# Performance work log

Hardware: AMD Instinct MI355X
Metric: run time of the kernel (lower is better)

The kernel has to match this reference:

```python
import jax, jax.numpy as jnp
import numpy as np

N_NODES = 50000
N_EDGES = 600000  # incidence entries; hyperedge ids also live in [0, N_NODES)
HID = 128


def _prelu(x, a):
    return jnp.where(x >= 0, x, a * x)


def _hypergraph_conv(x, W, b, node_idx, edge_idx, num_nodes, num_hedges):
    # PyG HypergraphConv (use_attention=False, heads=1):
    # out = D^{-1} H B^{-1} H^T (X Theta) + bias
    xw = x @ W  # [N, F]
    ones = jnp.ones(node_idx.shape[0], dtype=x.dtype)
    D = jax.ops.segment_sum(ones, node_idx, num_segments=num_nodes)   # node degree
    B = jax.ops.segment_sum(ones, edge_idx, num_segments=num_hedges)  # hyperedge degree
    Dinv = jnp.where(D > 0, 1.0 / D, 0.0)
    Binv = jnp.where(B > 0, 1.0 / B, 0.0)
    # node -> hyperedge aggregation, scaled by B^{-1}
    m = jax.ops.segment_sum(xw[node_idx], edge_idx, num_segments=num_hedges) * Binv[:, None]
    # hyperedge -> node aggregation, scaled by D^{-1}
    out = jax.ops.segment_sum(m[edge_idx], node_idx, num_segments=num_nodes) * Dinv[:, None]
    return out + b


def setup_inputs() -> dict:
    key = jax.random.key(0)
    k1, k2, k3, k4, k5 = jax.random.split(key, 5)
    x = jax.random.normal(k1, (N_NODES, HID), dtype=jnp.float32)
    hyper_edge_index = jax.random.randint(k2, (2, N_EDGES), 0, N_NODES, dtype=jnp.int64)
    # kaiming-normal-ish linear weights, zero biases (per init_weights)
    std = float(np.sqrt(2.0 / HID))
    W1 = jax.random.normal(k3, (HID, HID), dtype=jnp.float32) * std
    W2 = jax.random.normal(k4, (HID, HID), dtype=jnp.float32) * std
    b1 = jnp.zeros((HID,), dtype=jnp.float32)
    b2 = jnp.zeros((HID,), dtype=jnp.float32)
    prelu_a = jnp.full((1,), 0.25, dtype=jnp.float32)  # nn.PReLU default
    return {"x": x, "hyper_edge_index": hyper_edge_index,
            "W1": W1, "b1": b1, "W2": W2, "b2": b2, "prelu_a": prelu_a}


def reference(x, hyper_edge_index, W1, b1, W2, b2, prelu_a):
    node_idx = hyper_edge_index[0]
    edge_idx = hyper_edge_index[1]
    h = _hypergraph_conv(x, W1, b1, node_idx, edge_idx, N_NODES, N_NODES)
    h = _prelu(h, prelu_a)
    h = _hypergraph_conv(h, W2, b2, node_idx, edge_idx, N_NODES, N_NODES)
    h = h + x  # residual
    return _prelu(h, prelu_a)
```

## Files before the change

kernel.cpp:

```cpp
#include <hip/hip_runtime.h>

typedef unsigned short u16;
typedef unsigned int   u32;
typedef unsigned long long u64;

#define HID 128
#define KPB 256
#define NBMAX 512
#define IPB 2048
#define CAP 6144

typedef __bf16 bf16x8 __attribute__((ext_vector_type(8)));
typedef float  f32x4  __attribute__((ext_vector_type(4)));

__device__ inline float u2f(u32 u){ union{u32 u;float f;} v; v.u=u; return v.f; }
__device__ inline u32   f2u(float f){ union{float f;u32 u;} v; v.f=f; return v.u; }
__device__ inline u32  f2bfu(float f){ u32 b=f2u(f); return ((b + 0x7FFFu + ((b>>16)&1u))>>16)&0xFFFFu; }
__device__ inline float blo(u32 u){ return u2f(u<<16); }
__device__ inline float bhi(u32 u){ return u2f(u & 0xFFFF0000u); }
__device__ inline u32  pk(float lo, float hi){ return (f2bfu(hi)<<16) | f2bfu(lo); }

__global__ __launch_bounds__(256) void k_wfrag2(const float* __restrict__ W1, const float* __restrict__ W2,
                                                u16* __restrict__ W1f, u16* __restrict__ W2f){
    int gid = blockIdx.x*256 + threadIdx.x;
    const float* W = (gid < 16384) ? W1 : W2;
    u16* Wf = (gid < 16384) ? W1f : W2f;
    int id = gid & 16383;
    int i = id & 7, l = (id>>3)&63, j = (id>>9)&7, s = id>>12;
    int k = s*32 + ((l>>4)<<3) + i;
    int n = (j<<4) + (l&15);
    Wf[id] = (u16)f2bfu(W[k*HID + n]);
}

__global__ __launch_bounds__(256) void k_hist(const int* __restrict__ nidx, const int* __restrict__ eidx,
                                              int* __restrict__ hist, int nE, int nN, int nb){
    __shared__ int h[NBMAX];
    for (int t=threadIdx.x; t<nb; t+=256) h[t]=0;
    __syncthreads();
    int base = blockIdx.x*IPB;
    for (int k=threadIdx.x; k<IPB; k+=256){
        int j = base+k;
        if (j < nE){
            int n = nidx[j], e = eidx[j];
            atomicAdd(&h[n>>8], 1);
            atomicAdd(&h[(nN+e)>>8], 1);
        }
    }
    __syncthreads();
    for (int t=threadIdx.x; t<nb; t+=256) if (h[t]) atomicAdd(&hist[t], h[t]);
}

__global__ __launch_bounds__(256) void k_bscan(const int* __restrict__ hist, int* __restrict__ bbase,
                                               int* __restrict__ bfill, int* __restrict__ off,
                                               int nb, int nkeys, int total){
    __shared__ int sd[256];
    int t = threadIdx.x;
    int c0 = (2*t   < nb) ? hist[2*t]   : 0;
    int c1 = (2*t+1 < nb) ? hist[2*t+1] : 0;
    int s = c0 + c1;
    sd[t] = s; __syncthreads();
    for (int o=1;o<256;o<<=1){ int u = (t>=o)? sd[t-o] : 0; __syncthreads(); sd[t]+=u; __syncthreads(); }
    int ex = sd[t] - s;
    if (2*t   < nb){ bbase[2*t]   = ex;      bfill[2*t]   = ex; }
    if (2*t+1 < nb){ bbase[2*t+1] = ex+c0;   bfill[2*t+1] = ex+c0; }
    if (t == 0){ bbase[nb] = total; off[nkeys] = total; }
}

__global__ __launch_bounds__(256) void k_part(const int* __restrict__ nidx, const int* __restrict__ eidx,
                                              int* __restrict__ bfill, u64* __restrict__ pairs,
                                              int nE, int nN, int nb){
    __shared__ int h[NBMAX], rsv[NBMAX], fl[NBMAX];
    for (int t=threadIdx.x; t<nb; t+=256){ h[t]=0; fl[t]=0; }
    __syncthreads();
    int base = blockIdx.x*IPB;
    for (int k=threadIdx.x; k<IPB; k+=256){
        int j = base+k;
        if (j < nE){
            int n = nidx[j], e = eidx[j];
            atomicAdd(&h[n>>8], 1);
            atomicAdd(&h[(nN+e)>>8], 1);
        }
    }
    __syncthreads();
    for (int t=threadIdx.x; t<nb; t+=256){ if (h[t]) rsv[t] = atomicAdd(&bfill[t], h[t]); }
    __syncthreads();
    for (int k=threadIdx.x; k<IPB; k+=256){
        int j = base+k;
        if (j < nE){
            int n = nidx[j], e = eidx[j];
            int b1 = n>>8;
            int p1 = rsv[b1] + atomicAdd(&fl[b1], 1);
            pairs[p1] = ((u64)(u32)n << 32) | (u32)e;
            int k2 = nN + e;
            int b2 = k2>>8;
            int p2 = rsv[b2] + atomicAdd(&fl[b2], 1);
            pairs[p2] = ((u64)(u32)k2 << 32) | (u32)n;
        }
    }
}

__global__ __launch_bounds__(256) void k_bucket(const u64* __restrict__ pairs, const int* __restrict__ bbase,
                                                int* __restrict__ csr, int* __restrict__ off, int nkeys){
    __shared__ int cntS[KPB];
    __shared__ int fillS[KPB];
    __shared__ int vals[CAP];
    int b = blockIdx.x;
    int t = threadIdx.x;
    int base = bbase[b];
    int n = bbase[b+1] - base;
    int k0 = b * KPB;

    cntS[t] = 0;
    __syncthreads();
    for (int i=t; i<n; i+=256){
        u64 p = pairs[base+i];
        int kl = (int)(p>>32) - k0;
        atomicAdd(&cntS[kl], 1);
    }
    __syncthreads();
    int c = cntS[t];
    __syncthreads();
    fillS[t] = c; __syncthreads();
    for (int o=1;o<256;o<<=1){ int u = (t>=o)? fillS[t-o] : 0; __syncthreads(); fillS[t]+=u; __syncthreads(); }
    int ex = fillS[t] - c;
    __syncthreads();
    cntS[t] = ex; fillS[t] = ex;
    __syncthreads();
    int k = k0 + t;
    if (k < nkeys) off[k] = base + ex;
    bool fits = (n <= CAP);
    for (int i=t; i<n; i+=256){
        u64 p = pairs[base+i];
        int kl = (int)(p>>32) - k0;
        int pos = atomicAdd(&fillS[kl], 1);
        if (fits) vals[pos] = (int)(u32)p;
        else      csr[base+pos] = (int)(u32)p;
    }
    __syncthreads();
    if (fits){
        for (int i=t; i<n; i+=256) csr[base+i] = vals[i];
    }
}

__global__ __launch_bounds__(256) void k_gemm(const u16* __restrict__ A, const u16* __restrict__ Wf,
                                              u16* __restrict__ C, int M){
    int wave = blockIdx.x*4 + (threadIdx.x>>6);
    int lane = threadIdx.x & 63;
    int rtiles = M >> 4;
    if (wave >= rtiles) return;
    int row0 = wave << 4;

    const u16* Arow = A + (size_t)(row0 + (lane&15))*HID + ((lane>>4)<<3);
    const bf16x8* Wp = reinterpret_cast<const bf16x8*>(Wf) + lane;

    f32x4 acc[8];
    #pragma unroll
    for (int j=0;j<8;++j) acc[j] = (f32x4){0.f,0.f,0.f,0.f};

    #pragma unroll
    for (int s=0;s<4;++s){
        bf16x8 a = *reinterpret_cast<const bf16x8*>(Arow + s*32);
        #pragma unroll
        for (int j=0;j<8;++j){
            bf16x8 b = Wp[(s*8 + j)*64];
            acc[j] = __builtin_amdgcn_mfma_f32_16x16x32_bf16(a, b, acc[j], 0, 0, 0);
        }
    }
    int r0 = row0 + ((lane>>4)<<2);
    int c0 = lane & 15;
    #pragma unroll
    for (int j=0;j<8;++j){
        #pragma unroll
        for (int r=0;r<4;++r){
            C[(size_t)(r0+r)*HID + j*16 + c0] = (u16)f2bfu(acc[j][r]);
        }
    }
}

__global__ __launch_bounds__(256) void k_gemm_f32(const float* __restrict__ A, const u16* __restrict__ Wf,
                                                  u16* __restrict__ C, int M){
    int wave = blockIdx.x*4 + (threadIdx.x>>6);
    int lane = threadIdx.x & 63;
    int rtiles = M >> 4;
    if (wave >= rtiles) return;
    int row0 = wave << 4;

    const float* Arow = A + (size_t)(row0 + (lane&15))*HID + ((lane>>4)<<3);
    const bf16x8* Wp = reinterpret_cast<const bf16x8*>(Wf) + lane;

    f32x4 acc[8];
    #pragma unroll
    for (int j=0;j<8;++j) acc[j] = (f32x4){0.f,0.f,0.f,0.f};

    #pragma unroll
    for (int s=0;s<4;++s){
        float4 f0 = *reinterpret_cast<const float4*>(Arow + s*32);
        float4 f1 = *reinterpret_cast<const float4*>(Arow + s*32 + 4);
        union { u16 h[8]; bf16x8 v; } au;
        au.h[0]=(u16)f2bfu(f0.x); au.h[1]=(u16)f2bfu(f0.y); au.h[2]=(u16)f2bfu(f0.z); au.h[3]=(u16)f2bfu(f0.w);
        au.h[4]=(u16)f2bfu(f1.x); au.h[5]=(u16)f2bfu(f1.y); au.h[6]=(u16)f2bfu(f1.z); au.h[7]=(u16)f2bfu(f1.w);
        #pragma unroll
        for (int j=0;j<8;++j){
            bf16x8 b = Wp[(s*8 + j)*64];
            acc[j] = __builtin_amdgcn_mfma_f32_16x16x32_bf16(au.v, b, acc[j], 0, 0, 0);
        }
    }
    int r0 = row0 + ((lane>>4)<<2);
    int c0 = lane & 15;
    #pragma unroll
    for (int j=0;j<8;++j){
        #pragma unroll
        for (int r=0;r<4;++r){
            C[(size_t)(r0+r)*HID + j*16 + c0] = (u16)f2bfu(acc[j][r]);
        }
    }
}

template<int MODE>
__global__ __launch_bounds__(256) void k_agg(const u32* __restrict__ tab, const int* __restrict__ csr,
                                             const int* __restrict__ off, void* __restrict__ outp,
                                             const float* __restrict__ bias, const float* __restrict__ resid,
                                             const float* __restrict__ aptr, int nrows){
    int d = blockIdx.x*4 + (threadIdx.x>>6);
    if (d >= nrows) return;
    int lane = threadIdx.x & 63;
    int g = lane >> 4;
    int c = lane & 15;
    int start = off[d], end = off[d+1];
    int deg = end - start;

    int myc = 0;
    if (lane < deg) myc = csr[start + lane];

    float a0=0.f,a1=0.f,a2=0.f,a3=0.f,a4=0.f,a5=0.f,a6=0.f,a7=0.f;
    int nb4 = deg < 64 ? deg : 64;
    for (int jb = 0; jb < nb4; jb += 4){
        int j = jb + g;
        int src = __shfl(myc, j, 64);
        uint4 v = make_uint4(0u,0u,0u,0u);
        if (j < nb4) v = *reinterpret_cast<const uint4*>(tab + (size_t)src*64 + (c<<2));
        a0 += blo(v.x); a1 += bhi(v.x);
        a2 += blo(v.y); a3 += bhi(v.y);
        a4 += blo(v.z); a5 += bhi(v.z);
        a6 += blo(v.w); a7 += bhi(v.w);
    }
    for (int j = start + 64; j < end; ++j){
        uint4 v = make_uint4(0u,0u,0u,0u);
        if (g == 0){
            int src = csr[j];
            v = *reinterpret_cast<const uint4*>(tab + (size_t)src*64 + (c<<2));
        }
        a0 += blo(v.x); a1 += bhi(v.x);
        a2 += blo(v.y); a3 += bhi(v.y);
        a4 += blo(v.z); a5 += bhi(v.z);
        a6 += blo(v.w); a7 += bhi(v.w);
    }
    a0 += __shfl_xor(a0,16,64); a0 += __shfl_xor(a0,32,64);
    a1 += __shfl_xor(a1,16,64); a1 += __shfl_xor(a1,32,64);
    a2 += __shfl_xor(a2,16,64); a2 += __shfl_xor(a2,32,64);
    a3 += __shfl_xor(a3,16,64); a3 += __shfl_xor(a3,32,64);
    a4 += __shfl_xor(a4,16,64); a4 += __shfl_xor(a4,32,64);
    a5 += __shfl_xor(a5,16,64); a5 += __shfl_xor(a5,32,64);
    a6 += __shfl_xor(a6,16,64); a6 += __shfl_xor(a6,32,64);
    a7 += __shfl_xor(a7,16,64); a7 += __shfl_xor(a7,32,64);

    if (g == 0){
        float s = (deg > 0) ? 1.0f/(float)deg : 0.f;
        a0*=s; a1*=s; a2*=s; a3*=s; a4*=s; a5*=s; a6*=s; a7*=s;
        if constexpr (MODE >= 1){
            float4 b0 = *reinterpret_cast<const float4*>(bias + (c<<3));
            float4 b1v = *reinterpret_cast<const float4*>(bias + (c<<3) + 4);
            a0+=b0.x; a1+=b0.y; a2+=b0.z; a3+=b0.w;
            a4+=b1v.x; a5+=b1v.y; a6+=b1v.z; a7+=b1v.w;
        }
        if constexpr (MODE == 2){
            const float* rp = resid + (size_t)d*HID + (c<<3);
            float4 r0 = *reinterpret_cast<const float4*>(rp);
            float4 r1 = *reinterpret_cast<const float4*>(rp + 4);
            a0+=r0.x; a1+=r0.y; a2+=r0.z; a3+=r0.w;
            a4+=r1.x; a5+=r1.y; a6+=r1.z; a7+=r1.w;
        }
        if constexpr (MODE >= 1){
            float al = aptr[0];
            a0 = (a0>=0.f)? a0 : al*a0;  a1 = (a1>=0.f)? a1 : al*a1;
            a2 = (a2>=0.f)? a2 : al*a2;  a3 = (a3>=0.f)? a3 : al*a3;
            a4 = (a4>=0.f)? a4 : al*a4;  a5 = (a5>=0.f)? a5 : al*a5;
            a6 = (a6>=0.f)? a6 : al*a6;  a7 = (a7>=0.f)? a7 : al*a7;
        }
        if constexpr (MODE == 2){
            float* op = (float*)outp + (size_t)d*HID + (c<<3);
            *reinterpret_cast<float4*>(op)     = make_float4(a0,a1,a2,a3);
            *reinterpret_cast<float4*>(op + 4) = make_float4(a4,a5,a6,a7);
        } else {
            uint4 wv;
            wv.x = pk(a0,a1); wv.y = pk(a2,a3); wv.z = pk(a4,a5); wv.w = pk(a6,a7);
            *reinterpret_cast<uint4*>((u32*)outp + (size_t)d*64 + (c<<2)) = wv;
        }
    }
}

extern "C" void kernel_launch(void* const* d_in, const int* in_sizes, int n_in,
                              void* d_out, int out_size, void* d_ws, size_t ws_size,
                              hipStream_t stream){
    (void)n_in; (void)out_size; (void)ws_size;
    const float* x  = (const float*)d_in[0];
    const int*  hei = (const int*)  d_in[1];
    const float* W1 = (const float*)d_in[2];
    const float* b1 = (const float*)d_in[3];
    const float* W2 = (const float*)d_in[4];
    const float* b2 = (const float*)d_in[5];
    const float* ap = (const float*)d_in[6];

    const int nN = in_sizes[0] / HID;
    const int nE = in_sizes[1] / 2;
    const int* nidx = hei;
    const int* eidx = hei + nE;
    const int nkeys = 2*nN;
    const int nb    = (nkeys + KPB - 1) / KPB;

    char* w = (char*)d_ws;
    size_t o = 0;
    auto alloc = [&](size_t bytes)->void*{
        void* p = (void*)(w + o);
        o += (bytes + 255) & ~(size_t)255;
        return p;
    };
    int* hist  = (int*)alloc((size_t)NBMAX*sizeof(int));
    int* bbase = (int*)alloc((size_t)(NBMAX+1)*sizeof(int));
    int* bfill = (int*)alloc((size_t)NBMAX*sizeof(int));
    int* off   = (int*)alloc(((size_t)nkeys+1)*sizeof(int));
    int* csr   = (int*)alloc((size_t)2*nE*sizeof(int));
    u64* pairs = (u64*)alloc((size_t)2*nE*sizeof(u64));
    u16* hb    = (u16*)alloc((size_t)nN*HID*sizeof(u16));
    u16* bufB  = (u16*)alloc((size_t)nN*HID*sizeof(u16));
    u16* bufC  = (u16*)alloc((size_t)nN*HID*sizeof(u16));
    u16* w1f   = (u16*)alloc((size_t)HID*HID*sizeof(u16));
    u16* w2f   = (u16*)alloc((size_t)HID*HID*sizeof(u16));

    hipMemsetAsync(hist, 0, (size_t)nb*sizeof(int), stream);

    k_wfrag2<<<128, 256, 0, stream>>>(W1, W2, w1f, w2f);

    const int rtiles = nN/16;
    const int ggrid  = (rtiles + 3)/4;
    k_gemm_f32<<<ggrid, 256, 0, stream>>>(x, w1f, bufB, nN);

    const int pgrid = (nE + IPB - 1)/IPB;
    k_hist <<<pgrid, 256, 0, stream>>>(nidx, eidx, hist, nE, nN, nb);
    k_bscan<<<1,     256, 0, stream>>>(hist, bbase, bfill, off, nb, nkeys, 2*nE);
    k_part <<<pgrid, 256, 0, stream>>>(nidx, eidx, bfill, pairs, nE, nN, nb);
    k_bucket<<<nb,   256, 0, stream>>>(pairs, bbase, csr, off, nkeys);

    const int agrid  = (nN + 3)/4;

    k_agg<0><<<agrid, 256, 0, stream>>>((const u32*)bufB, csr, off + nN, bufC, nullptr, nullptr, nullptr, nN);
    k_agg<1><<<agrid, 256, 0, stream>>>((const u32*)bufC, csr, off,      hb,   b1, nullptr, ap, nN);
    k_gemm<<<ggrid, 256, 0, stream>>>(hb, w2f, bufB, nN);
    k_agg<0><<<agrid, 256, 0, stream>>>((const u32*)bufB, csr, off + nN, bufC, nullptr, nullptr, nullptr, nN);
    k_agg<2><<<agrid, 256, 0, stream>>>((const u32*)bufC, csr, off, d_out, b2, x, ap, nN);
}
```

Baseline: 253.2 us.

## Fold memset and bucket scan into neighbouring kernels; unroll aggregation gather

Removes the hipMemsetAsync and the single-block k_bscan launch. Their work moves into k_wfrag2, which now zeroes hist and bfill, and into k_part and k_bucket, which each recompute the bucket prefix scan redundantly per block from the global histogram. bfill becomes a per-bucket fill counter starting at zero instead of an absolute base. Separately, the first-64-neighbour gather loop in k_agg is unrolled by four so each lane issues four independent row loads before accumulating. This trades redundant per-block scan work and more registers for fewer launches and more memory-level parallelism.

```diff
diff --git a/kernel.cpp b/kernel.cpp
--- a/kernel.cpp
+++ b/kernel.cpp
@@ -21,8 +21,12 @@
 __device__ inline u32  pk(float lo, float hi){ return (f2bfu(hi)<<16) | f2bfu(lo); }
 
 __global__ __launch_bounds__(256) void k_wfrag2(const float* __restrict__ W1, const float* __restrict__ W2,
-                                                u16* __restrict__ W1f, u16* __restrict__ W2f){
+                                                u16* __restrict__ W1f, u16* __restrict__ W2f,
+                                                int* __restrict__ hist, int* __restrict__ bfill,
+                                                int* __restrict__ off, int nkeys, int total){
     int gid = blockIdx.x*256 + threadIdx.x;
+    if (gid < NBMAX){ hist[gid] = 0; bfill[gid] = 0; }
+    if (gid == 0) off[nkeys] = total;
     const float* W = (gid < 16384) ? W1 : W2;
     u16* Wf = (gid < 16384) ? W1f : W2f;
     int id = gid & 16383;
@@ -50,41 +54,34 @@
     for (int t=threadIdx.x; t<nb; t+=256) if (h[t]) atomicAdd(&hist[t], h[t]);
 }
 
-__global__ __launch_bounds__(256) void k_bscan(const int* __restrict__ hist, int* __restrict__ bbase,
-                                               int* __restrict__ bfill, int* __restrict__ off,
-                                               int nb, int nkeys, int total){
-    __shared__ int sd[256];
+__global__ __launch_bounds__(256) void k_part(const int* __restrict__ nidx, const int* __restrict__ eidx,
+                                              const int* __restrict__ hist, int* __restrict__ bfill,
+                                              u64* __restrict__ pairs, int nE, int nN, int nb){
+    __shared__ int h[NBMAX], rsv[NBMAX], fl[NBMAX], bb[NBMAX], sd[256];
     int t = threadIdx.x;
+    for (int i=t; i<nb; i+=256){ h[i]=0; fl[i]=0; }
+    __syncthreads();
+    int base = blockIdx.x*IPB;
+    for (int k=t; k<IPB; k+=256){
+        int j = base+k;
+        if (j < nE){
+            int n = nidx[j], e = eidx[j];
+            atomicAdd(&h[n>>8], 1);
+            atomicAdd(&h[(nN+e)>>8], 1);
+        }
+    }
     int c0 = (2*t   < nb) ? hist[2*t]   : 0;
     int c1 = (2*t+1 < nb) ? hist[2*t+1] : 0;
     int s = c0 + c1;
     sd[t] = s; __syncthreads();
     for (int o=1;o<256;o<<=1){ int u = (t>=o)? sd[t-o] : 0; __syncthreads(); sd[t]+=u; __syncthreads(); }
     int ex = sd[t] - s;
-    if (2*t   < nb){ bbase[2*t]   = ex;      bfill[2*t]   = ex; }
-    if (2*t+1 < nb){ bbase[2*t+1] = ex+c0;   bfill[2*t+1] = ex+c0; }
-    if (t == 0){ bbase[nb] = total; off[nkeys] = total; }
-}
-
-__global__ __launch_bounds__(256) void k_part(const int* __restrict__ nidx, const int* __restrict__ eidx,
-                                              int* __restrict__ bfill, u64* __restrict__ pairs,
-                                              int nE, int nN, int nb){
-    __shared__ int h[NBMAX], rsv[NBMAX], fl[NBMAX];
-    for (int t=threadIdx.x; t<nb; t+=256){ h[t]=0; fl[t]=0; }
-    __syncthreads();
-    int base = blockIdx.x*IPB;
-    for (int k=threadIdx.x; k<IPB; k+=256){
-        int j = base+k;
-        if (j < nE){
-            int n = nidx[j], e = eidx[j];
-            atomicAdd(&h[n>>8], 1);
-            atomicAdd(&h[(nN+e)>>8], 1);
-        }
-    }
-    __syncthreads();
-    for (int t=threadIdx.x; t<nb; t+=256){ if (h[t]) rsv[t] = atomicAdd(&bfill[t], h[t]); }
-    __syncthreads();
-    for (int k=threadIdx.x; k<IPB; k+=256){
+    if (2*t   < nb) bb[2*t]   = ex;
+    if (2*t+1 < nb) bb[2*t+1] = ex + c0;
+    __syncthreads();
+    for (int i=t; i<nb; i+=256){ if (h[i]) rsv[i] = bb[i] + atomicAdd(&bfill[i], h[i]); }
+    __syncthreads();
+    for (int k=t; k<IPB; k+=256){
         int j = base+k;
         if (j < nE){
             int n = nidx[j], e = eidx[j];
@@ -99,15 +96,27 @@
     }
 }
 
-__global__ __launch_bounds__(256) void k_bucket(const u64* __restrict__ pairs, const int* __restrict__ bbase,
-                                                int* __restrict__ csr, int* __restrict__ off, int nkeys){
+__global__ __launch_bounds__(256) void k_bucket(const u64* __restrict__ pairs, const int* __restrict__ hist,
+                                                int* __restrict__ csr, int* __restrict__ off,
+                                                int nkeys, int nb){
     __shared__ int cntS[KPB];
     __shared__ int fillS[KPB];
+    __shared__ int bbS[NBMAX+1];
+    __shared__ int sd[256];
     __shared__ int vals[CAP];
     int b = blockIdx.x;
     int t = threadIdx.x;
-    int base = bbase[b];
-    int n = bbase[b+1] - base;
+    int c0 = (2*t   < nb) ? hist[2*t]   : 0;
+    int c1 = (2*t+1 < nb) ? hist[2*t+1] : 0;
+    int s = c0 + c1;
+    sd[t] = s; __syncthreads();
+    for (int o=1;o<256;o<<=1){ int u = (t>=o)? sd[t-o] : 0; __syncthreads(); sd[t]+=u; __syncthreads(); }
+    int ex = sd[t] - s;
+    if (2*t   <= nb) bbS[2*t]   = ex;
+    if (2*t+1 <= nb) bbS[2*t+1] = ex + c0;
+    __syncthreads();
+    int base = bbS[b];
+    int n = bbS[b+1] - base;
     int k0 = b * KPB;
 
     cntS[t] = 0;
@@ -122,12 +131,12 @@
     __syncthreads();
     fillS[t] = c; __syncthreads();
     for (int o=1;o<256;o<<=1){ int u = (t>=o)? fillS[t-o] : 0; __syncthreads(); fillS[t]+=u; __syncthreads(); }
-    int ex = fillS[t] - c;
-    __syncthreads();
-    cntS[t] = ex; fillS[t] = ex;
+    int ex2 = fillS[t] - c;
+    __syncthreads();
+    cntS[t] = ex2; fillS[t] = ex2;
     __syncthreads();
     int k = k0 + t;
-    if (k < nkeys) off[k] = base + ex;
+    if (k < nkeys) off[k] = base + ex2;
     bool fits = (n <= CAP);
     for (int i=t; i<n; i+=256){
         u64 p = pairs[base+i];
@@ -234,15 +243,25 @@
 
     float a0=0.f,a1=0.f,a2=0.f,a3=0.f,a4=0.f,a5=0.f,a6=0.f,a7=0.f;
     int nb4 = deg < 64 ? deg : 64;
-    for (int jb = 0; jb < nb4; jb += 4){
-        int j = jb + g;
-        int src = __shfl(myc, j, 64);
-        uint4 v = make_uint4(0u,0u,0u,0u);
-        if (j < nb4) v = *reinterpret_cast<const uint4*>(tab + (size_t)src*64 + (c<<2));
-        a0 += blo(v.x); a1 += bhi(v.x);
-        a2 += blo(v.y); a3 += bhi(v.y);
-        a4 += blo(v.z); a5 += bhi(v.z);
-        a6 += blo(v.w); a7 += bhi(v.w);
+    for (int jb = 0; jb < nb4; jb += 16){
+        int j0 = jb + g, j1 = jb + 4 + g, j2 = jb + 8 + g, j3 = jb + 12 + g;
+        int s0 = __shfl(myc, j0, 64);
+        int s1 = __shfl(myc, j1, 64);
+        int s2 = __shfl(myc, j2, 64);
+        int s3 = __shfl(myc, j3, 64);
+        uint4 v0 = make_uint4(0u,0u,0u,0u), v1 = v0, v2 = v0, v3 = v0;
+        if (j0 < nb4) v0 = *reinterpret_cast<const uint4*>(tab + (size_t)s0*64 + (c<<2));
+        if (j1 < nb4) v1 = *reinterpret_cast<const uint4*>(tab + (size_t)s1*64 + (c<<2));
+        if (j2 < nb4) v2 = *reinterpret_cast<const uint4*>(tab + (size_t)s2*64 + (c<<2));
+        if (j3 < nb4) v3 = *reinterpret_cast<const uint4*>(tab + (size_t)s3*64 + (c<<2));
+        a0 += blo(v0.x)+blo(v1.x)+blo(v2.x)+blo(v3.x);
+        a1 += bhi(v0.x)+bhi(v1.x)+bhi(v2.x)+bhi(v3.x);
+        a2 += blo(v0.y)+blo(v1.y)+blo(v2.y)+blo(v3.y);
+        a3 += bhi(v0.y)+bhi(v1.y)+bhi(v2.y)+bhi(v3.y);
+        a4 += blo(v0.z)+blo(v1.z)+blo(v2.z)+blo(v3.z);
+        a5 += bhi(v0.z)+bhi(v1.z)+bhi(v2.z)+bhi(v3.z);
+        a6 += blo(v0.w)+blo(v1.w)+blo(v2.w)+blo(v3.w);
+        a7 += bhi(v0.w)+bhi(v1.w)+bhi(v2.w)+bhi(v3.w);
     }
     for (int j = start + 64; j < end; ++j){
         uint4 v = make_uint4(0u,0u,0u,0u);
@@ -326,7 +345,6 @@
         return p;
     };
     int* hist  = (int*)alloc((size_t)NBMAX*sizeof(int));
-    int* bbase = (int*)alloc((size_t)(NBMAX+1)*sizeof(int));
     int* bfill = (int*)alloc((size_t)NBMAX*sizeof(int));
     int* off   = (int*)alloc(((size_t)nkeys+1)*sizeof(int));
     int* csr   = (int*)alloc((size_t)2*nE*sizeof(int));
@@ -337,19 +355,16 @@
     u16* w1f   = (u16*)alloc((size_t)HID*HID*sizeof(u16));
     u16* w2f   = (u16*)alloc((size_t)HID*HID*sizeof(u16));
 
-    hipMemsetAsync(hist, 0, (size_t)nb*sizeof(int), stream);
-
-    k_wfrag2<<<128, 256, 0, stream>>>(W1, W2, w1f, w2f);
+    k_wfrag2<<<128, 256, 0, stream>>>(W1, W2, w1f, w2f, hist, bfill, off, nkeys, 2*nE);
 
     const int rtiles = nN/16;
     const int ggrid  = (rtiles + 3)/4;
     k_gemm_f32<<<ggrid, 256, 0, stream>>>(x, w1f, bufB, nN);
 
     const int pgrid = (nE + IPB - 1)/IPB;
-    k_hist <<<pgrid, 256, 0, stream>>>(nidx, eidx, hist, nE, nN, nb);
-    k_bscan<<<1,     256, 0, stream>>>(hist, bbase, bfill, off, nb, nkeys, 2*nE);
-    k_part <<<pgrid, 256, 0, stream>>>(nidx, eidx, bfill, pairs, nE, nN, nb);
-    k_bucket<<<nb,   256, 0, stream>>>(pairs, bbase, csr, off, nkeys);
+    k_hist  <<<pgrid, 256, 0, stream>>>(nidx, eidx, hist, nE, nN, nb);
+    k_part  <<<pgrid, 256, 0, stream>>>(nidx, eidx, hist, bfill, pairs, nE, nN, nb);
+    k_bucket<<<nb,    256, 0, stream>>>(pairs, hist, csr, off, nkeys, nb);
 
     const int agrid  = (nN + 3)/4;
 
```

New measurement: 239.8 us. -5.3%, faster.
